# Optimization experiments

Hardware: AMD Instinct MI355X
Metric: run time of the kernel (lower is better)

The kernel has to match this reference:

```python
import jax, jax.numpy as jnp
import numpy as np

BS, HID, INP, SPAN, OUT, DAYS = 32768, 128, 64, 8, 2, 20


def _init(key, shape, fan_in):
    # mimic torch default uniform(-1/sqrt(fan), 1/sqrt(fan)) init
    bound = 1.0 / np.sqrt(fan_in)
    return jax.random.uniform(key, shape, jnp.float32, -bound, bound)


def setup_inputs() -> dict:
    key = jax.random.key(0)
    ks = jax.random.split(key, 11)
    return {
        "hx": jax.random.normal(ks[0], (BS, HID), jnp.float32),
        # GRUCell params (PyTorch layout: gates stacked [r, z, n])
        "w_ih": _init(ks[1], (3 * HID, INP), HID),
        "w_hh": _init(ks[2], (3 * HID, HID), HID),
        "b_ih": _init(ks[3], (3 * HID,), HID),
        "b_hh": _init(ks[4], (3 * HID,), HID),
        # fc_in: hid -> input
        "fc_in_w": _init(ks[5], (INP, HID), HID),
        "fc_in_b": _init(ks[6], (INP,), HID),
        # fc_out: hid -> out
        "fc_out_w": _init(ks[7], (OUT, HID), HID),
        "fc_out_b": _init(ks[8], (OUT,), HID),
        # num_span_layer: hid -> num_span_classes
        "span_w": _init(ks[9], (SPAN, HID), HID),
        "span_b": _init(ks[10], (SPAN,), HID),
    }


def _gru_cell(x, h, w_ih, w_hh, b_ih, b_hh):
    gi = x @ w_ih.T + b_ih  # [B, 3H]
    gh = h @ w_hh.T + b_hh  # [B, 3H]
    i_r, i_z, i_n = jnp.split(gi, 3, axis=-1)
    h_r, h_z, h_n = jnp.split(gh, 3, axis=-1)
    r = jax.nn.sigmoid(i_r + h_r)
    z = jax.nn.sigmoid(i_z + h_z)
    n = jnp.tanh(i_n + r * h_n)
    return (1.0 - z) * n + z * h


def reference(hx, w_ih, w_hh, b_ih, b_hh, fc_in_w, fc_in_b,
              fc_out_w, fc_out_b, span_w, span_b):
    num_spans = jax.nn.softmax(hx @ span_w.T + span_b, axis=-1)  # [B, SPAN]
    x0 = jnp.zeros((hx.shape[0], fc_in_w.shape[0]), hx.dtype)  # zero first input

    def step(carry, _):
        h, x = carry
        h = _gru_cell(x, h, w_ih, w_hh, b_ih, b_hh)
        x = jax.nn.relu(h @ fc_in_w.T + fc_in_b)
        out = jax.nn.softmax(h @ fc_out_w.T + fc_out_b, axis=-1)  # [B, OUT]
        return (h, x), out

    _, outs = jax.lax.scan(step, (hx, x0), None, length=DAYS)  # [DAYS, B, OUT]
    outputs = jnp.transpose(outs, (1, 0, 2))  # [B, DAYS, OUT]
    return num_spans, outputs
```

## Files before the change

kernel.cpp:

```cpp
#include <hip/hip_runtime.h>
#include <hip/hip_bf16.h>

#define HID 128
#define INP 64
#define SPANN 8
#define NOUT 2
#define DAYS 20
#define RT 4
#define ROWS (16*RT)
#define NTH 512

typedef __attribute__((ext_vector_type(8))) short short8;
typedef __attribute__((ext_vector_type(4))) float f32x4;
typedef __attribute__((ext_vector_type(2))) float f32x2;
typedef unsigned int u32;
typedef __attribute__((ext_vector_type(2))) u32 u32x2;
typedef unsigned short u16;

#define MFMA(a,b,c) __builtin_amdgcn_mfma_f32_16x16x32_bf16(a,b,c,0,0,0)
#define RCPF(x)  __builtin_amdgcn_rcpf(x)
#define EXP2F(x) __builtin_amdgcn_exp2f(x)
#define LOG2E  1.4426950408889634f
#define LOG2E2 2.8853900817779268f

__device__ __forceinline__ u32 pack2(float a, float b){
    __hip_bfloat162 h = __float22bfloat162_rn(float2{a, b});
    u32 r; __builtin_memcpy(&r, &h, 4); return r;
}
__device__ __forceinline__ float sigf(float x){
    return RCPF(1.0f + EXP2F(-LOG2E * x));
}
__device__ __forceinline__ float tanhf_(float x){
    return fmaf(-2.0f, RCPF(1.0f + EXP2F(LOG2E2 * x)), 1.0f);
}

union frag_u { short8 s; u32 w[4]; };
__device__ __forceinline__ short8 ldfrag(const float* p){
    const f32x4 a = *(const f32x4*)p;
    const f32x4 b = *(const f32x4*)(p+4);
    frag_u f;
    f.w[0] = pack2(a[0],a[1]); f.w[1] = pack2(a[2],a[3]);
    f.w[2] = pack2(b[0],b[1]); f.w[3] = pack2(b[2],b[3]);
    return f.s;
}


__global__ __launch_bounds__(NTH, 2) void gru_mfma(
    const float* __restrict__ hx, const float* __restrict__ w_ih,
    const float* __restrict__ w_hh, const float* __restrict__ b_ih,
    const float* __restrict__ b_hh, const float* __restrict__ fc_in_w,
    const float* __restrict__ fc_in_b, const float* __restrict__ fc_out_w,
    const float* __restrict__ fc_out_b, const float* __restrict__ span_w,
    const float* __restrict__ span_b, float* __restrict__ out, int bs)
{
    __shared__ u16 hL[2][RT*2048];
    __shared__ u16 xL[2][RT*1024];

    const int tid = threadIdx.x;
    const int wid = tid >> 6;
    const int l   = tid & 63;
    const int r15 = l & 15;
    const int hi  = l >> 4;
    const int row0 = blockIdx.x * ROWS;

    short8 whhR[4], whhZ[4], whhN[4];
    short8 wihR[2], wihZ[2], wihN[2];
    short8 fwA[4];
    const int g0 = wid*16 + r15;
    #pragma unroll
    for (int ks = 0; ks < 4; ++ks){
        whhR[ks] = ldfrag(w_hh + (size_t)(      g0)*HID + ks*32 + hi*8);
        whhZ[ks] = ldfrag(w_hh + (size_t)(128 + g0)*HID + ks*32 + hi*8);
        whhN[ks] = ldfrag(w_hh + (size_t)(256 + g0)*HID + ks*32 + hi*8);
    }
    #pragma unroll
    for (int ks = 0; ks < 2; ++ks){
        wihR[ks] = ldfrag(w_ih + (size_t)(      g0)*INP + ks*32 + hi*8);
        wihZ[ks] = ldfrag(w_ih + (size_t)(128 + g0)*INP + ks*32 + hi*8);
        wihN[ks] = ldfrag(w_ih + (size_t)(256 + g0)*INP + ks*32 + hi*8);
    }
    {
        const short8 zz = {0,0,0,0,0,0,0,0};
        #pragma unroll
        for (int ks = 0; ks < 4; ++ks){
            if (wid < 4)            fwA[ks] = ldfrag(fc_in_w + (size_t)(wid*16 + r15)*HID + ks*32 + hi*8);
            else if (wid == 4)      fwA[ks] = (r15 < NOUT) ? ldfrag(fc_out_w + (size_t)r15*HID + ks*32 + hi*8) : zz;
            else                    fwA[ks] = zz;
        }
    }

    f32x4 bRv, bZv, bNiv, bNhv, fbv;
    #pragma unroll
    for (int q = 0; q < 4; ++q){
        const int g = wid*16 + hi*4 + q;
        bRv[q]  = b_ih[g]       + b_hh[g];
        bZv[q]  = b_ih[128 + g] + b_hh[128 + g];
        bNiv[q] = b_ih[256 + g];
        bNhv[q] = b_hh[256 + g];
        if (wid < 4)       fbv[q] = fc_in_b[wid*16 + hi*4 + q];
        else if (wid == 4) fbv[q] = (hi == 0 && q < NOUT) ? fc_out_b[q] : 0.0f;
        else               fbv[q] = 0.0f;
    }

    const int wu32 = (wid>>1)*256 + (((wid&1)*2 + (hi>>1))*16 + r15)*4 + (hi&1)*2;

    float hOld[RT][4];
    const int c0 = wid*16 + hi*4;
    #pragma unroll
    for (int rt = 0; rt < RT; ++rt){
        const f32x4 h4 = *(const f32x4*)(hx + (size_t)(row0 + rt*16 + r15)*HID + c0);
        #pragma unroll
        for (int q = 0; q < 4; ++q) hOld[rt][q] = h4[q];
        u32x2 wv; wv[0] = pack2(h4[0], h4[1]); wv[1] = pack2(h4[2], h4[3]);
        *(u32x2*)((u32*)&hL[0][rt*2048] + wu32) = wv;
    }
    {
        u32* xb = (u32*)&xL[0][0];
        for (int i = tid; i < RT*512; i += NTH) xb[i] = 0u;
    }
    __syncthreads();

    if (wid == 5){
        const short8 zz = {0,0,0,0,0,0,0,0};
        short8 spw[4];
        #pragma unroll
        for (int ks = 0; ks < 4; ++ks)
            spw[ks] = (r15 < SPANN) ? ldfrag(span_w + (size_t)r15*HID + ks*32 + hi*8) : zz;
        f32x4 sb = {0.0f, 0.0f, 0.0f, 0.0f};
        #pragma unroll
        for (int q = 0; q < 4; ++q) if (hi < 2) sb[q] = span_b[hi*4 + q];
        #pragma unroll
        for (int rt = 0; rt < RT; ++rt){
            const short8* hf = (const short8*)&hL[0][rt*2048];
            f32x4 acc = sb;
            #pragma unroll
            for (int ks = 0; ks < 4; ++ks) acc = MFMA(spw[ks], hf[ks*64 + l], acc);
            if (hi < 2){
                float m = fmaxf(fmaxf(acc[0], acc[1]), fmaxf(acc[2], acc[3]));
                m = fmaxf(m, __shfl_xor(m, 16));
                float e0 = EXP2F(LOG2E*(acc[0]-m)), e1 = EXP2F(LOG2E*(acc[1]-m));
                float e2 = EXP2F(LOG2E*(acc[2]-m)), e3 = EXP2F(LOG2E*(acc[3]-m));
                float s = e0 + e1 + e2 + e3;
                s += __shfl_xor(s, 16);
                const float inv = RCPF(s);
                f32x4 o = {e0*inv, e1*inv, e2*inv, e3*inv};
                *(f32x4*)(out + (size_t)(row0 + rt*16 + r15)*SPANN + hi*4) = o;
            }
        }
    }

    float* __restrict__ outp = out + (size_t)bs * SPANN;

    #pragma unroll 2
    for (int day = 0; day < DAYS; ++day){
        const int p = day & 1;
        const u16* hRd = hL[p];
        const u16* xRd = xL[p];
        u32* hWr = (u32*)hL[p^1];
        u32* xWr = (u32*)xL[p^1];

        #pragma unroll
        for (int rt = 0; rt < RT; ++rt){
            const short8* hf = (const short8*)(hRd + rt*2048);
            const short8* xf = (const short8*)(xRd + rt*1024);
            const short8 h0 = hf[l], h1 = hf[64+l], h2 = hf[128+l], h3 = hf[192+l];
            const short8 x0 = xf[l], x1 = xf[64+l];

            f32x4 aR  = MFMA(whhR[0], h0, bRv);
            f32x4 aZ  = MFMA(whhZ[0], h0, bZv);
            f32x4 aNh = MFMA(whhN[0], h0, bNhv);
            aR  = MFMA(whhR[1], h1, aR);  aZ  = MFMA(whhZ[1], h1, aZ);  aNh = MFMA(whhN[1], h1, aNh);
            aR  = MFMA(whhR[2], h2, aR);  aZ  = MFMA(whhZ[2], h2, aZ);  aNh = MFMA(whhN[2], h2, aNh);
            aR  = MFMA(whhR[3], h3, aR);  aZ  = MFMA(whhZ[3], h3, aZ);  aNh = MFMA(whhN[3], h3, aNh);
            f32x4 aNi = MFMA(wihN[0], x0, bNiv);
            aR  = MFMA(wihR[0], x0, aR);  aZ  = MFMA(wihZ[0], x0, aZ);
            aNi = MFMA(wihN[1], x1, aNi);
            aR  = MFMA(wihR[1], x1, aR);  aZ  = MFMA(wihZ[1], x1, aZ);

            float hn[4];
            #pragma unroll
            for (int q = 0; q < 4; ++q){
                const float rg = sigf(aR[q]);
                const float zg = sigf(aZ[q]);
                const float nn = tanhf_(fmaf(rg, aNh[q], aNi[q]));
                hn[q] = fmaf(zg, hOld[rt][q] - nn, nn);
                hOld[rt][q] = hn[q];
            }
            u32x2 wv; wv[0] = pack2(hn[0], hn[1]); wv[1] = pack2(hn[2], hn[3]);
            *(u32x2*)(hWr + rt*1024 + wu32) = wv;
        }
        __syncthreads();

        if (wid < 4){
            #pragma unroll
            for (int rt = 0; rt < RT; ++rt){
                const short8* hf = (const short8*)(hL[p^1] + rt*2048);
                const short8 h0 = hf[l], h1 = hf[64+l], h2 = hf[128+l], h3 = hf[192+l];
                f32x4 ax = MFMA(fwA[0], h0, fbv);
                ax = MFMA(fwA[1], h1, ax);
                ax = MFMA(fwA[2], h2, ax);
                ax = MFMA(fwA[3], h3, ax);
                u32x2 wv;
                wv[0] = pack2(fmaxf(ax[0],0.0f), fmaxf(ax[1],0.0f));
                wv[1] = pack2(fmaxf(ax[2],0.0f), fmaxf(ax[3],0.0f));
                *(u32x2*)(xWr + rt*512 + wu32) = wv;
            }
        } else if (wid == 4){
            #pragma unroll
            for (int rt = 0; rt < RT; ++rt){
                const short8* hf = (const short8*)(hL[p^1] + rt*2048);
                const short8 h0 = hf[l], h1 = hf[64+l], h2 = hf[128+l], h3 = hf[192+l];
                f32x4 ao = MFMA(fwA[0], h0, fbv);
                ao = MFMA(fwA[1], h1, ao);
                ao = MFMA(fwA[2], h2, ao);
                ao = MFMA(fwA[3], h3, ao);
                if (hi == 0){
                    const float m  = fmaxf(ao[0], ao[1]);
                    const float e0 = EXP2F(LOG2E*(ao[0]-m));
                    const float e1 = EXP2F(LOG2E*(ao[1]-m));
                    const float inv = RCPF(e0 + e1);
                    f32x2 o = {e0*inv, e1*inv};
                    *(f32x2*)(outp + ((size_t)(row0 + rt*16 + r15)*DAYS + day)*NOUT) = o;
                }
            }
        }
        __syncthreads();
    }
}

extern "C" void kernel_launch(void* const* d_in, const int* in_sizes, int n_in,
                              void* d_out, int out_size, void* d_ws, size_t ws_size,
                              hipStream_t stream) {
    const float* hx       = (const float*)d_in[0];
    const float* w_ih     = (const float*)d_in[1];
    const float* w_hh     = (const float*)d_in[2];
    const float* b_ih     = (const float*)d_in[3];
    const float* b_hh     = (const float*)d_in[4];
    const float* fc_in_w  = (const float*)d_in[5];
    const float* fc_in_b  = (const float*)d_in[6];
    const float* fc_out_w = (const float*)d_in[7];
    const float* fc_out_b = (const float*)d_in[8];
    const float* span_w   = (const float*)d_in[9];
    const float* span_b   = (const float*)d_in[10];
    float* out = (float*)d_out;

    const int bs = in_sizes[0] / HID;
    dim3 grid(bs / ROWS), block(NTH);
    gru_mfma<<<grid, block, 0, stream>>>(hx, w_ih, w_hh, b_ih, b_hh,
                                         fc_in_w, fc_in_b, fc_out_w, fc_out_b,
                                         span_w, span_b, out, bs);
}
```

Measured before the change: 149.7 us.

## Pipeline fc_in across half-tiles, fold 2-way softmax into sigmoid of dot-product difference

The day loop is restructured so each half of the row tiles runs the GRU update, then the fc_in projection for the other half runs on all eight waves, with a single x buffer. This replaces the phase where only waves 0-4 worked while the rest idled. The two-class output softmax becomes a sigmoid of a logit difference, computed as partial dot products in the GRU epilogue and reduced through shared memory by one wave. fc_in weights move from registers to LDS to free registers, and the span softmax is split across four waves. The tighter schedule relies on careful buffer aliasing and adds extra LDS traffic.

```diff
diff --git a/kernel.cpp b/kernel.cpp
--- a/kernel.cpp
+++ b/kernel.cpp
@@ -27,12 +27,8 @@
     __hip_bfloat162 h = __float22bfloat162_rn(float2{a, b});
     u32 r; __builtin_memcpy(&r, &h, 4); return r;
 }
-__device__ __forceinline__ float sigf(float x){
-    return RCPF(1.0f + EXP2F(-LOG2E * x));
-}
-__device__ __forceinline__ float tanhf_(float x){
-    return fmaf(-2.0f, RCPF(1.0f + EXP2F(LOG2E2 * x)), 1.0f);
-}
+__device__ __forceinline__ float sigf(float x){ return RCPF(1.0f + EXP2F(-LOG2E * x)); }
+__device__ __forceinline__ float tanhf_(float x){ return fmaf(-2.0f, RCPF(1.0f + EXP2F(LOG2E2 * x)), 1.0f); }
 
 union frag_u { short8 s; u32 w[4]; };
 __device__ __forceinline__ short8 ldfrag(const float* p){
@@ -54,7 +50,9 @@
     const float* __restrict__ span_b, float* __restrict__ out, int bs)
 {
     __shared__ u16 hL[2][RT*2048];
-    __shared__ u16 xL[2][RT*1024];
+    __shared__ u16 xL[RT*1024];
+    __shared__ u16 finL[4*4*64*8];
+    __shared__ __attribute__((aligned(16))) float diffP[ROWS][8];
 
     const int tid = threadIdx.x;
     const int wid = tid >> 6;
@@ -62,10 +60,11 @@
     const int r15 = l & 15;
     const int hi  = l >> 4;
     const int row0 = blockIdx.x * ROWS;
+    const int mB  = wid & 3;
+    const int rtB_off = wid >> 2;
 
     short8 whhR[4], whhZ[4], whhN[4];
     short8 wihR[2], wihZ[2], wihN[2];
-    short8 fwA[4];
     const int g0 = wid*16 + r15;
     #pragma unroll
     for (int ks = 0; ks < 4; ++ks){
@@ -79,153 +78,149 @@
         wihZ[ks] = ldfrag(w_ih + (size_t)(128 + g0)*INP + ks*32 + hi*8);
         wihN[ks] = ldfrag(w_ih + (size_t)(256 + g0)*INP + ks*32 + hi*8);
     }
-    {
-        const short8 zz = {0,0,0,0,0,0,0,0};
-        #pragma unroll
-        for (int ks = 0; ks < 4; ++ks){
-            if (wid < 4)            fwA[ks] = ldfrag(fc_in_w + (size_t)(wid*16 + r15)*HID + ks*32 + hi*8);
-            else if (wid == 4)      fwA[ks] = (r15 < NOUT) ? ldfrag(fc_out_w + (size_t)r15*HID + ks*32 + hi*8) : zz;
-            else                    fwA[ks] = zz;
-        }
-    }
-
-    f32x4 bRv, bZv, bNiv, bNhv, fbv;
+
+    for (int s = tid; s < 1024; s += NTH) {
+        const int mt = s >> 8, ks = (s >> 6) & 3, ll = s & 63;
+        short8 f = ldfrag(fc_in_w + (size_t)(mt*16 + (ll&15))*HID + ks*32 + (ll>>4)*8);
+        *((short8*)finL + s) = f;
+    }
+
+    f32x4 bRv, bZv, bNiv, bNhv, fbv, wd4;
+    const int c0 = wid*16 + hi*4;
     #pragma unroll
     for (int q = 0; q < 4; ++q){
-        const int g = wid*16 + hi*4 + q;
+        const int g = c0 + q;
         bRv[q]  = b_ih[g]       + b_hh[g];
         bZv[q]  = b_ih[128 + g] + b_hh[128 + g];
         bNiv[q] = b_ih[256 + g];
         bNhv[q] = b_hh[256 + g];
-        if (wid < 4)       fbv[q] = fc_in_b[wid*16 + hi*4 + q];
-        else if (wid == 4) fbv[q] = (hi == 0 && q < NOUT) ? fc_out_b[q] : 0.0f;
-        else               fbv[q] = 0.0f;
-    }
-
-    const int wu32 = (wid>>1)*256 + (((wid&1)*2 + (hi>>1))*16 + r15)*4 + (hi&1)*2;
-
-    float hOld[RT][4];
-    const int c0 = wid*16 + hi*4;
-    #pragma unroll
-    for (int rt = 0; rt < RT; ++rt){
-        const f32x4 h4 = *(const f32x4*)(hx + (size_t)(row0 + rt*16 + r15)*HID + c0);
-        #pragma unroll
-        for (int q = 0; q < 4; ++q) hOld[rt][q] = h4[q];
-        u32x2 wv; wv[0] = pack2(h4[0], h4[1]); wv[1] = pack2(h4[2], h4[3]);
-        *(u32x2*)((u32*)&hL[0][rt*2048] + wu32) = wv;
-    }
+        fbv[q]  = fc_in_b[mB*16 + hi*4 + q];
+        wd4[q]  = fc_out_w[g] - fc_out_w[HID + g];
+    }
+    const float bd = fc_out_b[0] - fc_out_b[1];
+
+    const int wu32  = (wid>>1)*256 + (((wid&1)*2 + (hi>>1))*16 + r15)*4 + (hi&1)*2;
+    const int xwu32 = (mB >>1)*256 + (((mB &1)*2 + (hi>>1))*16 + r15)*4 + (hi&1)*2;
+
+    f32x4 hOld0, hOld1, hOld2, hOld3;
     {
-        u32* xb = (u32*)&xL[0][0];
+        #define LOADH(RTG, HO) do { \
+            const f32x4 h4 = *(const f32x4*)(hx + (size_t)(row0 + (RTG)*16 + r15)*HID + c0); \
+            HO = h4; \
+            u32x2 wv; wv[0] = pack2(h4[0], h4[1]); wv[1] = pack2(h4[2], h4[3]); \
+            *(u32x2*)((u32*)&hL[0][(RTG)*2048] + wu32) = wv; } while(0)
+        LOADH(0, hOld0); LOADH(1, hOld1); LOADH(2, hOld2); LOADH(3, hOld3);
+        #undef LOADH
+        u32* xb = (u32*)&xL[0];
         for (int i = tid; i < RT*512; i += NTH) xb[i] = 0u;
     }
     __syncthreads();
 
-    if (wid == 5){
+    if (wid < 4){
         const short8 zz = {0,0,0,0,0,0,0,0};
         short8 spw[4];
         #pragma unroll
         for (int ks = 0; ks < 4; ++ks)
             spw[ks] = (r15 < SPANN) ? ldfrag(span_w + (size_t)r15*HID + ks*32 + hi*8) : zz;
-        f32x4 sb = {0.0f, 0.0f, 0.0f, 0.0f};
+        f32x4 acc = {0.f,0.f,0.f,0.f};
         #pragma unroll
-        for (int q = 0; q < 4; ++q) if (hi < 2) sb[q] = span_b[hi*4 + q];
+        for (int q = 0; q < 4; ++q) if (hi < 2) acc[q] = span_b[hi*4 + q];
+        const short8* hf = (const short8*)&hL[0][wid*2048];
         #pragma unroll
-        for (int rt = 0; rt < RT; ++rt){
-            const short8* hf = (const short8*)&hL[0][rt*2048];
-            f32x4 acc = sb;
-            #pragma unroll
-            for (int ks = 0; ks < 4; ++ks) acc = MFMA(spw[ks], hf[ks*64 + l], acc);
-            if (hi < 2){
-                float m = fmaxf(fmaxf(acc[0], acc[1]), fmaxf(acc[2], acc[3]));
-                m = fmaxf(m, __shfl_xor(m, 16));
-                float e0 = EXP2F(LOG2E*(acc[0]-m)), e1 = EXP2F(LOG2E*(acc[1]-m));
-                float e2 = EXP2F(LOG2E*(acc[2]-m)), e3 = EXP2F(LOG2E*(acc[3]-m));
-                float s = e0 + e1 + e2 + e3;
-                s += __shfl_xor(s, 16);
-                const float inv = RCPF(s);
-                f32x4 o = {e0*inv, e1*inv, e2*inv, e3*inv};
-                *(f32x4*)(out + (size_t)(row0 + rt*16 + r15)*SPANN + hi*4) = o;
-            }
+        for (int ks = 0; ks < 4; ++ks) acc = MFMA(spw[ks], hf[ks*64 + l], acc);
+        if (hi < 2){
+            float m = fmaxf(fmaxf(acc[0], acc[1]), fmaxf(acc[2], acc[3]));
+            m = fmaxf(m, __shfl_xor(m, 16));
+            float e0 = EXP2F(LOG2E*(acc[0]-m)), e1 = EXP2F(LOG2E*(acc[1]-m));
+            float e2 = EXP2F(LOG2E*(acc[2]-m)), e3 = EXP2F(LOG2E*(acc[3]-m));
+            float s = e0 + e1 + e2 + e3;
+            s += __shfl_xor(s, 16);
+            const float inv = RCPF(s);
+            f32x4 o = {e0*inv, e1*inv, e2*inv, e3*inv};
+            *(f32x4*)(out + (size_t)(row0 + wid*16 + r15)*SPANN + hi*4) = o;
         }
     }
 
     float* __restrict__ outp = out + (size_t)bs * SPANN;
 
+    #define TILE_A(RTG, hRd_, hWr_, HO) do { \
+        const short8* hf = (const short8*)((hRd_) + (RTG)*2048); \
+        const short8* xf = (const short8*)(xL + (RTG)*1024); \
+        const short8 h0=hf[l], h1=hf[64+l], h2=hf[128+l], h3=hf[192+l]; \
+        const short8 x0=xf[l], x1=xf[64+l]; \
+        f32x4 aR  = MFMA(whhR[0], h0, bRv); \
+        f32x4 aZ  = MFMA(whhZ[0], h0, bZv); \
+        f32x4 aNh = MFMA(whhN[0], h0, bNhv); \
+        aR = MFMA(whhR[1],h1,aR); aZ = MFMA(whhZ[1],h1,aZ); aNh = MFMA(whhN[1],h1,aNh); \
+        aR = MFMA(whhR[2],h2,aR); aZ = MFMA(whhZ[2],h2,aZ); aNh = MFMA(whhN[2],h2,aNh); \
+        aR = MFMA(whhR[3],h3,aR); aZ = MFMA(whhZ[3],h3,aZ); aNh = MFMA(whhN[3],h3,aNh); \
+        f32x4 aNi = MFMA(wihN[0], x0, bNiv); \
+        aR = MFMA(wihR[0],x0,aR); aZ = MFMA(wihZ[0],x0,aZ); \
+        aNi = MFMA(wihN[1],x1,aNi); \
+        aR = MFMA(wihR[1],x1,aR); aZ = MFMA(wihZ[1],x1,aZ); \
+        float hn[4]; \
+        _Pragma("unroll") for (int q=0;q<4;++q){ \
+            const float rg = sigf(aR[q]); const float zg = sigf(aZ[q]); \
+            const float nn = tanhf_(fmaf(rg, aNh[q], aNi[q])); \
+            hn[q] = fmaf(zg, HO[q]-nn, nn); HO[q] = hn[q]; } \
+        u32x2 wv; wv[0]=pack2(hn[0],hn[1]); wv[1]=pack2(hn[2],hn[3]); \
+        *(u32x2*)((hWr_) + (RTG)*1024 + wu32) = wv; \
+        float pd = hn[0]*wd4[0]; pd = fmaf(hn[1],wd4[1],pd); \
+        pd = fmaf(hn[2],wd4[2],pd); pd = fmaf(hn[3],wd4[3],pd); \
+        pd += __shfl_xor(pd, 16); pd += __shfl_xor(pd, 32); \
+        if (hi == 0) diffP[(RTG)*16 + r15][wid] = pd; \
+    } while(0)
+
+    #define OUT_STORE(d_, gb_) do { \
+        if (wid == 7 && l < 32) { \
+            const int rowIdx = (gb_)*32 + l; \
+            const f32x4 v0 = *(const f32x4*)&diffP[rowIdx][0]; \
+            const f32x4 v1 = *(const f32x4*)&diffP[rowIdx][4]; \
+            const float s = ((v0[0]+v0[1])+(v0[2]+v0[3])) + ((v1[0]+v1[1])+(v1[2]+v1[3])); \
+            const float p0 = sigf(s + bd); \
+            f32x2 o = {p0, 1.0f - p0}; \
+            *(f32x2*)(outp + ((size_t)(row0 + rowIdx)*DAYS + (d_))*NOUT) = o; \
+        } \
+    } while(0)
+
+    #define TILE_B(d_, gb_, hSrc) do { \
+        if ((d_) < DAYS-1) { \
+            const int rtB = 2*(gb_) + rtB_off; \
+            const short8* hf = (const short8*)((hSrc) + rtB*2048); \
+            const short8 h0=hf[l], h1=hf[64+l], h2=hf[128+l], h3=hf[192+l]; \
+            const short8* fp = (const short8*)finL + mB*256 + l; \
+            f32x4 ax = MFMA(fp[0],   h0, fbv); \
+            ax       = MFMA(fp[64],  h1, ax); \
+            ax       = MFMA(fp[128], h2, ax); \
+            ax       = MFMA(fp[192], h3, ax); \
+            u32x2 wv; \
+            wv[0] = pack2(fmaxf(ax[0],0.f), fmaxf(ax[1],0.f)); \
+            wv[1] = pack2(fmaxf(ax[2],0.f), fmaxf(ax[3],0.f)); \
+            *(u32x2*)((u32*)xL + rtB*512 + xwu32) = wv; \
+        } \
+        OUT_STORE(d_, gb_); \
+    } while(0)
+
     #pragma unroll 2
-    for (int day = 0; day < DAYS; ++day){
-        const int p = day & 1;
-        const u16* hRd = hL[p];
-        const u16* xRd = xL[p];
-        u32* hWr = (u32*)hL[p^1];
-        u32* xWr = (u32*)xL[p^1];
-
-        #pragma unroll
-        for (int rt = 0; rt < RT; ++rt){
-            const short8* hf = (const short8*)(hRd + rt*2048);
-            const short8* xf = (const short8*)(xRd + rt*1024);
-            const short8 h0 = hf[l], h1 = hf[64+l], h2 = hf[128+l], h3 = hf[192+l];
-            const short8 x0 = xf[l], x1 = xf[64+l];
-
-            f32x4 aR  = MFMA(whhR[0], h0, bRv);
-            f32x4 aZ  = MFMA(whhZ[0], h0, bZv);
-            f32x4 aNh = MFMA(whhN[0], h0, bNhv);
-            aR  = MFMA(whhR[1], h1, aR);  aZ  = MFMA(whhZ[1], h1, aZ);  aNh = MFMA(whhN[1], h1, aNh);
-            aR  = MFMA(whhR[2], h2, aR);  aZ  = MFMA(whhZ[2], h2, aZ);  aNh = MFMA(whhN[2], h2, aNh);
-            aR  = MFMA(whhR[3], h3, aR);  aZ  = MFMA(whhZ[3], h3, aZ);  aNh = MFMA(whhN[3], h3, aNh);
-            f32x4 aNi = MFMA(wihN[0], x0, bNiv);
-            aR  = MFMA(wihR[0], x0, aR);  aZ  = MFMA(wihZ[0], x0, aZ);
-            aNi = MFMA(wihN[1], x1, aNi);
-            aR  = MFMA(wihR[1], x1, aR);  aZ  = MFMA(wihZ[1], x1, aZ);
-
-            float hn[4];
-            #pragma unroll
-            for (int q = 0; q < 4; ++q){
-                const float rg = sigf(aR[q]);
-                const float zg = sigf(aZ[q]);
-                const float nn = tanhf_(fmaf(rg, aNh[q], aNi[q]));
-                hn[q] = fmaf(zg, hOld[rt][q] - nn, nn);
-                hOld[rt][q] = hn[q];
-            }
-            u32x2 wv; wv[0] = pack2(hn[0], hn[1]); wv[1] = pack2(hn[2], hn[3]);
-            *(u32x2*)(hWr + rt*1024 + wu32) = wv;
-        }
+    for (int d = 0; d < DAYS; ++d){
+        const u16* hRd = hL[d & 1];
+        u32*       hWr = (u32*)hL[(d & 1) ^ 1];
+
+        TILE_A(0, hRd, hWr, hOld0);
+        TILE_A(1, hRd, hWr, hOld1);
+        if (d > 0) TILE_B(d-1, 1, hRd);
         __syncthreads();
 
-        if (wid < 4){
-            #pragma unroll
-            for (int rt = 0; rt < RT; ++rt){
-                const short8* hf = (const short8*)(hL[p^1] + rt*2048);
-                const short8 h0 = hf[l], h1 = hf[64+l], h2 = hf[128+l], h3 = hf[192+l];
-                f32x4 ax = MFMA(fwA[0], h0, fbv);
-                ax = MFMA(fwA[1], h1, ax);
-                ax = MFMA(fwA[2], h2, ax);
-                ax = MFMA(fwA[3], h3, ax);
-                u32x2 wv;
-                wv[0] = pack2(fmaxf(ax[0],0.0f), fmaxf(ax[1],0.0f));
-                wv[1] = pack2(fmaxf(ax[2],0.0f), fmaxf(ax[3],0.0f));
-                *(u32x2*)(xWr + rt*512 + wu32) = wv;
-            }
-        } else if (wid == 4){
-            #pragma unroll
-            for (int rt = 0; rt < RT; ++rt){
-                const short8* hf = (const short8*)(hL[p^1] + rt*2048);
-                const short8 h0 = hf[l], h1 = hf[64+l], h2 = hf[128+l], h3 = hf[192+l];
-                f32x4 ao = MFMA(fwA[0], h0, fbv);
-                ao = MFMA(fwA[1], h1, ao);
-                ao = MFMA(fwA[2], h2, ao);
-                ao = MFMA(fwA[3], h3, ao);
-                if (hi == 0){
-                    const float m  = fmaxf(ao[0], ao[1]);
-                    const float e0 = EXP2F(LOG2E*(ao[0]-m));
-                    const float e1 = EXP2F(LOG2E*(ao[1]-m));
-                    const float inv = RCPF(e0 + e1);
-                    f32x2 o = {e0*inv, e1*inv};
-                    *(f32x2*)(outp + ((size_t)(row0 + rt*16 + r15)*DAYS + day)*NOUT) = o;
-                }
-            }
-        }
+        TILE_A(2, hRd, hWr, hOld2);
+        TILE_A(3, hRd, hWr, hOld3);
+        TILE_B(d, 0, (const u16*)hWr);
         __syncthreads();
     }
+    OUT_STORE(DAYS-1, 1);
+
+    #undef TILE_A
+    #undef TILE_B
+    #undef OUT_STORE
 }
 
 extern "C" void kernel_launch(void* const* d_in, const int* in_sizes, int n_in,
```

After: 143.9 us. -3.9%, faster.
